# Performance work log

Hardware: AMD Instinct MI355X
Metric: run time of the kernel (lower is better)

The kernel has to match this reference:

```python
import jax, jax.numpy as jnp
import numpy as np

B, T, C = 4, 2048, 2048
H, HD = 16, 128  # n_heads, head_dim; C == H*HD


def _rope_rotate(x, cos, sin):
    """x: [b,t,h,d]; cos/sin: [t, d//2]. Complex multiply on interleaved pairs,
    matching torch view_as_complex on reshape(..., -1, 2)."""
    xr = x[..., 0::2]  # real parts  [b,t,h,d/2]
    xi = x[..., 1::2]  # imag parts
    c = cos[None, :, None, :]
    s = sin[None, :, None, :]
    or_ = xr * c - xi * s
    oi_ = xr * s + xi * c
    # interleave back: [..., d/2, 2] -> [..., d]
    return jnp.stack([or_, oi_], axis=-1).reshape(x.shape)


def setup_inputs() -> dict:
    key = jax.random.key(0)
    ks = jax.random.split(key, 6)
    x = jax.random.normal(ks[0], (B, T, C), dtype=jnp.float32)
    # causal boolean mask: True = attend
    attn_mask = jnp.tril(jnp.ones((T, T), dtype=bool))
    # standard RoPE frequencies (theta=10000)
    inv_freq = 1.0 / (10000.0 ** (np.arange(0, HD, 2, dtype=np.float32) / HD))
    ang = np.arange(T, dtype=np.float32)[:, None] * inv_freq[None, :]  # [T, HD/2]
    rope_cos = jnp.asarray(np.cos(ang))
    rope_sin = jnp.asarray(np.sin(ang))
    sc = 1.0 / np.sqrt(C)
    Wq = jax.random.normal(ks[1], (C, C), dtype=jnp.float32) * sc
    Wk = jax.random.normal(ks[2], (C, C), dtype=jnp.float32) * sc
    Wv = jax.random.normal(ks[3], (C, C), dtype=jnp.float32) * sc
    Wp = jax.random.normal(ks[4], (C, C), dtype=jnp.float32) * sc
    return {"x": x, "attn_mask": attn_mask, "rope_cos": rope_cos,
            "rope_sin": rope_sin, "Wq": Wq, "Wk": Wk, "Wv": Wv, "Wp": Wp}


def reference(x, attn_mask, rope_cos, rope_sin, Wq, Wk, Wv, Wp):
    b, t, c = x.shape
    # QKV projections (nn.Linear: y = x @ W.T), reshape to heads
    q = jnp.einsum('btc,dc->btd', x, Wq).reshape(b, t, H, HD)
    k = jnp.einsum('btc,dc->btd', x, Wk).reshape(b, t, H, HD)
    v = jnp.einsum('btc,dc->btd', x, Wv).reshape(b, t, H, HD)
    # RoPE on q, k
    q = _rope_rotate(q, rope_cos[:t], rope_sin[:t])
    k = _rope_rotate(k, rope_cos[:t], rope_sin[:t])
    # SDPA with boolean mask, scale 1/sqrt(head_dim)
    scores = jnp.einsum('bqhd,bkhd->bhqk', q, k) / jnp.sqrt(jnp.asarray(HD, x.dtype))
    neg = jnp.finfo(scores.dtype).min
    scores = jnp.where(attn_mask[None, None, :t, :t], scores, neg)
    attn = jax.nn.softmax(scores, axis=-1)
    out = jnp.einsum('bhqk,bkhd->bqhd', attn, v).reshape(b, t, H * HD)
    return jnp.einsum('btd,cd->btc', out, Wp)
```

## Files before the change

kernel.cpp:

```cpp
#include <hip/hip_runtime.h>

#define B_    4
#define T_    2048
#define C_    2048
#define H_    16
#define HD_   128
#define LDQK  4096

typedef __attribute__((ext_vector_type(8))) short short8v;
typedef __attribute__((ext_vector_type(4))) float float4v;
typedef __attribute__((ext_vector_type(16))) float float16v;

typedef const __attribute__((address_space(1))) void* gld_src_t;
typedef __attribute__((address_space(3))) void* gld_dst_t;
#define GLDS16(g, l) __builtin_amdgcn_global_load_lds((gld_src_t)(g), (gld_dst_t)(l), 16, 0, 0)

__device__ __forceinline__ unsigned short f2bf(float f) {
  unsigned int u = __float_as_uint(f);
  u += 0x7fffu + ((u >> 16) & 1u);
  return (unsigned short)(u >> 16);
}
__device__ __forceinline__ float bf2f(unsigned short s) {
  return __uint_as_float(((unsigned int)s) << 16);
}
__device__ __forceinline__ unsigned int cvtpk_bf16(float lo, float hi) {
  unsigned int r;
  asm("v_cvt_pk_bf16_f32 %0, %1, %2" : "=v"(r) : "v"(lo), "v"(hi));
  return r;
}

__global__ void cvt_kernel(const float* __restrict__ src, unsigned short* __restrict__ dst, int n4) {
  int i = blockIdx.x * blockDim.x + threadIdx.x;
  if (i >= n4) return;
  float4 v = reinterpret_cast<const float4*>(src)[i];
  ushort4 o;
  o.x = f2bf(v.x); o.y = f2bf(v.y); o.z = f2bf(v.z); o.w = f2bf(v.w);
  reinterpret_cast<ushort4*>(dst)[i] = o;
}


#define ISSUE_HALF(MAT, HA, KT, CBUF)                                             \
  { const unsigned short* gp_ = (MAT) ? Bm : A;                                   \
    const size_t gb_ = (MAT) ? bbase : abase;                                     \
    _Pragma("unroll")                                                             \
    for (int i_ = 0; i_ < 2; ++i_) {                                              \
      int fo_ = (i_ * 512 + tid) * 16;                              \
      int rl_ = fo_ >> 7;                                            \
      int row_ = (HA) * 128 + rl_;                                                \
      int g_ = (fo_ >> 4) & 7;                                                    \
      int ce_ = ((g_ ^ (rl_ & 7)) << 3);              \
      GLDS16(gp_ + gb_ + (size_t)row_ * K + (KT) * 64 + ce_,                      \
             lds + (CBUF) * 65536 + (MAT) * 32768 + (HA) * 16384 + fo_);          \
    } }

#define RD_A(dst, MI, KK, CBUF)                                                   \
  { int row_ = wm * 128 + (MI) * 16 + lr;                                         \
    dst = *reinterpret_cast<const short8v*>(                                      \
        lds + (CBUF) * 65536 + row_ * 128 + (((KK) * 64 + lg * 16) ^ ((row_ & 7) << 4))); }

#define RD_B(dst, NI, KK, CBUF)                                                   \
  { int row_ = wn * 64 + (NI) * 16 + lr;                                          \
    dst = *reinterpret_cast<const short8v*>(                                      \
        lds + (CBUF) * 65536 + 32768 + row_ * 128 + (((KK) * 64 + lg * 16) ^ ((row_ & 7) << 4))); }

#define MFMA_BLOCK(MBASE, BV)                                                     \
  { __builtin_amdgcn_s_setprio(1);                                                \
    _Pragma("unroll")                                                             \
    for (int ni_ = 0; ni_ < 4; ++ni_) {                                           \
      acc[(MBASE)+0][ni_] = __builtin_amdgcn_mfma_f32_16x16x32_bf16(a0, BV[ni_], acc[(MBASE)+0][ni_], 0,0,0); \
      acc[(MBASE)+1][ni_] = __builtin_amdgcn_mfma_f32_16x16x32_bf16(a1, BV[ni_], acc[(MBASE)+1][ni_], 0,0,0); \
      acc[(MBASE)+2][ni_] = __builtin_amdgcn_mfma_f32_16x16x32_bf16(a2, BV[ni_], acc[(MBASE)+2][ni_], 0,0,0); \
      acc[(MBASE)+3][ni_] = __builtin_amdgcn_mfma_f32_16x16x32_bf16(a3, BV[ni_], acc[(MBASE)+3][ni_], 0,0,0); \
    }                                                                             \
    __builtin_amdgcn_s_setprio(0); }

#define FENCE asm volatile("" ::: "memory")

template<int MODE>
__global__ __launch_bounds__(512, 2)
void gemm256(const unsigned short* __restrict__ A, const unsigned short* __restrict__ Bm,
             void* __restrict__ Cout, int K, int NB, int ldc)
{
  extern __shared__ char lds[];
  const int tid = threadIdx.x;
  const int l = tid & 63, w = tid >> 6;
  const int lr = l & 15, lg = l >> 4;
  const int wm = w >> 2, wn = w & 3;

  const int nwg = (int)gridDim.x;
  const int orig = (int)blockIdx.x;
  const int qq = nwg >> 3, rr = nwg & 7;
  const int xcd = orig & 7, idx = orig >> 3;
  const int wg = (xcd < rr ? xcd * (qq + 1) : rr * (qq + 1) + (xcd - rr) * qq) + idx;
  const int bm = wg / NB, bn = wg % NB;

  const size_t abase = (size_t)bm * 256 * (size_t)K;
  const size_t bbase = (size_t)bn * 256 * (size_t)K;

  float4v acc[8][4];
  const float4v fz = {0.f, 0.f, 0.f, 0.f};
#pragma unroll
  for (int i = 0; i < 8; ++i)
#pragma unroll
    for (int j = 0; j < 4; ++j) acc[i][j] = fz;

  const int nk = K >> 6;

  ISSUE_HALF(1, 0, 0, 0)
  ISSUE_HALF(1, 1, 0, 0)
  ISSUE_HALF(0, 0, 0, 0)
  ISSUE_HALF(0, 1, 0, 0)
  ISSUE_HALF(1, 0, (nk > 1 ? 1 : 0), 1)
  asm volatile("s_waitcnt vmcnt(2)" ::: "memory");
  __builtin_amdgcn_s_barrier();
  FENCE;

  short8v a0, a1, a2, a3;
  short8v bv0[4], bv1[4];

  for (int t = 0; t < nk; ++t) {
    const int c = t & 1;
    const int t1 = (t + 1 < nk) ? t + 1 : t;
    const int t2 = (t + 2 < nk) ? t + 2 : t;

    RD_A(a0, 0, 0, c) RD_A(a1, 1, 0, c) RD_A(a2, 2, 0, c) RD_A(a3, 3, 0, c)
    RD_B(bv0[0], 0, 0, c) RD_B(bv0[1], 1, 0, c) RD_B(bv0[2], 2, 0, c) RD_B(bv0[3], 3, 0, c)
    ISSUE_HALF(1, 1, t1, c ^ 1)
    ISSUE_HALF(0, 0, t1, c ^ 1)
    FENCE;
    __builtin_amdgcn_s_barrier();
    MFMA_BLOCK(0, bv0)
    FENCE;
    __builtin_amdgcn_s_barrier();
    FENCE;

    RD_A(a0, 4, 0, c) RD_A(a1, 5, 0, c) RD_A(a2, 6, 0, c) RD_A(a3, 7, 0, c)
    ISSUE_HALF(0, 1, t1, c ^ 1)
    FENCE;
    __builtin_amdgcn_s_barrier();
    MFMA_BLOCK(4, bv0)
    FENCE;
    __builtin_amdgcn_s_barrier();
    FENCE;

    RD_A(a0, 0, 1, c) RD_A(a1, 1, 1, c) RD_A(a2, 2, 1, c) RD_A(a3, 3, 1, c)
    RD_B(bv1[0], 0, 1, c) RD_B(bv1[1], 1, 1, c) RD_B(bv1[2], 2, 1, c) RD_B(bv1[3], 3, 1, c)
    FENCE;
    __builtin_amdgcn_s_barrier();
    MFMA_BLOCK(0, bv1)
    FENCE;
    __builtin_amdgcn_s_barrier();
    FENCE;

    RD_A(a0, 4, 1, c) RD_A(a1, 5, 1, c) RD_A(a2, 6, 1, c) RD_A(a3, 7, 1, c)
    ISSUE_HALF(1, 0, t2, c)
    FENCE;
    __builtin_amdgcn_s_barrier();
    MFMA_BLOCK(4, bv1)
    FENCE;
    asm volatile("s_waitcnt vmcnt(2)" ::: "memory");
    __builtin_amdgcn_s_barrier();
    FENCE;
  }

  const int row0 = bm * 256 + wm * 128;
  const int col0 = bn * 256 + wn * 64;
  if (MODE == 2) {
    unsigned short* vtp = (unsigned short*)Cout;
#pragma unroll
    for (int mi = 0; mi < 8; ++mi)
#pragma unroll
      for (int ni = 0; ni < 4; ++ni) {
        int col = col0 + ni * 16 + lr;
        int hh = col >> 7, dd = col & 127;
        int row = row0 + mi * 16 + lg * 4;
        int bb = row >> 11, t0 = row & 2047;
        ushort4 o4;
        o4.x = f2bf(acc[mi][ni][0]); o4.y = f2bf(acc[mi][ni][1]);
        o4.z = f2bf(acc[mi][ni][2]); o4.w = f2bf(acc[mi][ni][3]);
        *reinterpret_cast<ushort4*>(vtp + (((size_t)(bb * 16 + hh)) << 18) + (((size_t)dd) << 11) + t0) = o4;
      }
  } else {
#pragma unroll
    for (int mi = 0; mi < 8; ++mi)
#pragma unroll
      for (int ni = 0; ni < 4; ++ni)
#pragma unroll
        for (int r2 = 0; r2 < 4; ++r2) {
          int row = row0 + mi * 16 + lg * 4 + r2;
          int col = col0 + ni * 16 + lr;
          float v = acc[mi][ni][r2];
          if (MODE == 1)
            ((unsigned short*)Cout)[(size_t)row * ldc + col] = f2bf(v);
          else
            ((float*)Cout)[(size_t)row * ldc + col] = v;
        }
  }
}

__global__ void rope_kernel(unsigned short* __restrict__ qk,
                            const float* __restrict__ cosb, const float* __restrict__ sinb)
{
  int i = blockIdx.x * blockDim.x + threadIdx.x;
  int seg = i & 15;
  int h   = (i >> 4) & (H_ - 1);
  int bt  = i >> 8;
  if (bt >= B_ * T_) return;
  int t = bt & (T_ - 1);

  float4 cv = *reinterpret_cast<const float4*>(cosb + t * 64 + seg * 4);
  float4 sv = *reinterpret_cast<const float4*>(sinb + t * 64 + seg * 4);
  float cc[4] = {cv.x, cv.y, cv.z, cv.w};
  float ss[4] = {sv.x, sv.y, sv.z, sv.w};

  size_t base = (size_t)bt * LDQK + h * HD_ + seg * 8;
#pragma unroll
  for (int qkx = 0; qkx < 2; ++qkx) {
    unsigned short* p = qk + base + qkx * 2048;
    uint4 u = *reinterpret_cast<uint4*>(p);
    unsigned int* uu = reinterpret_cast<unsigned int*>(&u);
#pragma unroll
    for (int j = 0; j < 4; ++j) {
      float xr = bf2f((unsigned short)(uu[j] & 0xffffu));
      float xi = bf2f((unsigned short)(uu[j] >> 16));
      float orr = xr * cc[j] - xi * ss[j];
      float oii = xr * ss[j] + xi * cc[j];
      uu[j] = (unsigned int)f2bf(orr) | ((unsigned int)f2bf(oii) << 16);
    }
    *reinterpret_cast<uint4*>(p) = u;
  }
}

__global__ __launch_bounds__(256, 2)
void attn_kernel(const unsigned short* __restrict__ qk,
                 const unsigned short* __restrict__ vt,
                 unsigned short* __restrict__ out)
{
  __shared__ unsigned short Kl[2][64 * 128];
  __shared__ unsigned short Vl[2][128 * 64];

  const int wg = (int)blockIdx.x;
  const int bh = ((wg >> 6) << 3) | (wg & 7);
  const int bx = (wg >> 3) & 7;
  const int b = bh >> 4, h = bh & 15;
  const int tid = threadIdx.x, w = tid >> 6, l = tid & 63;
  const int q32 = l & 31, hi = l >> 5;
  const size_t rowbase = (size_t)b * T_;
  const unsigned short* kbase = qk + rowbase * LDQK + 2048 + h * HD_;
  const unsigned short* vbase = vt + (size_t)bh * (HD_ * (size_t)T_);
  const float SC = 0.12754089f;
  const float16v z16 = {0.f,0.f,0.f,0.f,0.f,0.f,0.f,0.f,0.f,0.f,0.f,0.f,0.f,0.f,0.f,0.f};

#define STAGE(kv0_, bi_)                                                          \
  {                                                                               \
    _Pragma("unroll")                                                             \
    for (int i_ = 0; i_ < 4; ++i_) {                                              \
      int fo = (i_ * 256 + tid) * 16;                                             \
      int row = fo >> 8;                                                          \
      int cb = (fo & 255) ^ ((row & 15) << 4);                                    \
      GLDS16(kbase + (size_t)((kv0_) + row) * LDQK + (cb >> 1), (char*)Kl[bi_] + fo); \
    }                                                                             \
    _Pragma("unroll")                                                             \
    for (int i_ = 0; i_ < 4; ++i_) {                                              \
      int fo = (i_ * 256 + tid) * 16;                                             \
      int r6 = (fo >> 8) & 63;                                                    \
      int s_ = (fo >> 7) & 1;                                                     \
      int dd = r6 | ((s_ ^ ((r6 >> 3) & 1)) << 6);                                \
      int k16 = ((fo >> 4) & 7) ^ (dd & 7);                                       \
      GLDS16(vbase + (size_t)dd * T_ + (kv0_) + k16 * 8, (char*)Vl[bi_] + fo);    \
    }                                                                             \
  }

  for (int sel = 0; sel < 2; ++sel) {
    const int qt = sel ? bx : (15 - bx);
    const int q0w = qt * 128 + w * 32;
    const int qg = q0w + q32;

    short8v qf[8];
#pragma unroll
    for (int kf = 0; kf < 8; ++kf) {
      short8v t = *reinterpret_cast<const short8v*>(
          qk + (rowbase + q0w + q32) * (size_t)LDQK + h * HD_ + kf * 16 + hi * 8);
      short8v r;
#pragma unroll
      for (int e = 0; e < 8; ++e) r[e] = (short)f2bf(bf2f((unsigned short)t[e]) * SC);
      qf[kf] = r;
    }

    float16v o[4];
#pragma unroll
    for (int db = 0; db < 4; ++db) o[db] = z16;
    float m_run = -1e30f, lsum = 0.f;

    const int nkv = 2 * (qt + 1);

    STAGE(0, 0);
    __syncthreads();

    for (int tile = 0; tile < nkv; ++tile) {
      const int kv0 = tile * 64;
      const int bi = tile & 1;
      if (tile + 1 < nkv) STAGE((tile + 1) * 64, bi ^ 1);

      if (kv0 <= q0w + 31) {
        float16v stv[2];
        stv[0] = z16; stv[1] = z16;
        __builtin_amdgcn_s_setprio(1);
#pragma unroll
        for (int kb = 0; kb < 2; ++kb) {
          int key = kb * 32 + q32;
          int swz = (key & 15) << 4;
          int rbase = key * 256;
#pragma unroll
          for (int kf = 0; kf < 8; ++kf) {
            short8v ak = *reinterpret_cast<const short8v*>(
                (char*)Kl[bi] + rbase + ((kf * 32 + hi * 16) ^ swz));
            stv[kb] = __builtin_amdgcn_mfma_f32_32x32x16_bf16(ak, qf[kf], stv[kb], 0, 0, 0);
          }
        }
        __builtin_amdgcn_s_setprio(0);
        if (kv0 + 63 > q0w) {
#pragma unroll
          for (int kb = 0; kb < 2; ++kb)
#pragma unroll
            for (int r = 0; r < 16; ++r) {
              int key = kv0 + kb * 32 + (r & 3) + 8 * ((r >> 2) & 3) + 4 * hi;
              if (key > qg) stv[kb][r] = -1e30f;
            }
        }
        float t16[16];
#pragma unroll
        for (int r = 0; r < 16; ++r) t16[r] = fmaxf(stv[0][r], stv[1][r]);
#pragma unroll
        for (int s = 8; s >= 1; s >>= 1)
#pragma unroll
          for (int r = 0; r < s; ++r) t16[r] = fmaxf(t16[r], t16[r + s]);
        float pm = fmaxf(t16[0], __shfl_xor(t16[0], 32));

        if (!__all(pm <= m_run + 8.0f)) {
          float mn = fmaxf(m_run, pm);
          float fac = exp2f(m_run - mn);
          lsum *= fac;
          m_run = mn;
#pragma unroll
          for (int r = 0; r < 16; ++r) {
            int src = (r & 3) + 8 * ((r >> 2) & 3) + 4 * hi;
            float fr = __shfl(fac, src);
#pragma unroll
            for (int db = 0; db < 4; ++db) o[db][r] *= fr;
          }
        }
        {
          float s16[16];
#pragma unroll
          for (int r = 0; r < 16; ++r) {
            float p0 = exp2f(stv[0][r] - m_run);
            float p1 = exp2f(stv[1][r] - m_run);
            stv[0][r] = p0; stv[1][r] = p1;
            s16[r] = p0 + p1;
          }
#pragma unroll
          for (int s = 8; s >= 1; s >>= 1)
#pragma unroll
            for (int r = 0; r < s; ++r) s16[r] += s16[r + s];
          lsum += s16[0] + __shfl_xor(s16[0], 32);
        }
        unsigned int pw0[8], pw1[8], xw0[8], xw1[8];
#pragma unroll
        for (int j = 0; j < 8; ++j) {
          pw0[j] = cvtpk_bf16(stv[0][2 * j], stv[0][2 * j + 1]);
          pw1[j] = cvtpk_bf16(stv[1][2 * j], stv[1][2 * j + 1]);
        }
#pragma unroll
        for (int j = 0; j < 8; ++j) {
          xw0[j] = __shfl_xor(pw0[j], 32);
          xw1[j] = __shfl_xor(pw1[j], 32);
        }
        union UW { unsigned int u[4]; short8v v; };
        short8v pb[4];
        {
          UW a0, a1, c0, c1;
          a0.u[0] = hi ? xw0[2] : pw0[0];  a0.u[1] = hi ? xw0[3] : pw0[1];
          a0.u[2] = hi ? pw0[2] : xw0[0];  a0.u[3] = hi ? pw0[3] : xw0[1];
          a1.u[0] = hi ? xw0[6] : pw0[4];  a1.u[1] = hi ? xw0[7] : pw0[5];
          a1.u[2] = hi ? pw0[6] : xw0[4];  a1.u[3] = hi ? pw0[7] : xw0[5];
          c0.u[0] = hi ? xw1[2] : pw1[0];  c0.u[1] = hi ? xw1[3] : pw1[1];
          c0.u[2] = hi ? pw1[2] : xw1[0];  c0.u[3] = hi ? pw1[3] : xw1[1];
          c1.u[0] = hi ? xw1[6] : pw1[4];  c1.u[1] = hi ? xw1[7] : pw1[5];
          c1.u[2] = hi ? pw1[6] : xw1[4];  c1.u[3] = hi ? pw1[7] : xw1[5];
          pb[0] = a0.v; pb[1] = a1.v; pb[2] = c0.v; pb[3] = c1.v;
        }
        __builtin_amdgcn_s_setprio(1);
#pragma unroll
        for (int db = 0; db < 4; ++db) {
          int dd = db * 32 + q32;
          int rb2 = (dd & 63) * 256 + ((((dd >> 6) ^ ((dd >> 3) & 1)) & 1) << 7);
          int swz = (dd & 7) << 4;
#pragma unroll
          for (int kb16 = 0; kb16 < 4; ++kb16) {
            short8v bv = *reinterpret_cast<const short8v*>(
                (char*)Vl[bi] + rb2 + ((kb16 * 32 + hi * 16) ^ swz));
            o[db] = __builtin_amdgcn_mfma_f32_32x32x16_bf16(pb[kb16], bv, o[db], 0, 0, 0);
          }
        }
        __builtin_amdgcn_s_setprio(0);
      }
      __syncthreads();
    }

    float linv = 1.0f / lsum;
#pragma unroll
    for (int r = 0; r < 16; ++r) {
      int src = (r & 3) + 8 * ((r >> 2) & 3) + 4 * hi;
      float lr_ = __shfl(linv, src);
      size_t rowoff = (rowbase + q0w + src) * (size_t)C_ + h * HD_ + q32;
#pragma unroll
      for (int db = 0; db < 4; ++db)
        out[rowoff + db * 32] = f2bf(o[db][r] * lr_);
    }
  }
#undef STAGE
}

extern "C" void kernel_launch(void* const* d_in, const int* in_sizes, int n_in,
                              void* d_out, int out_size, void* d_ws, size_t ws_size,
                              hipStream_t stream) {
  (void)in_sizes; (void)n_in; (void)out_size; (void)ws_size;
  const float* x  = (const float*)d_in[0];
  const float* rc = (const float*)d_in[2];
  const float* rs = (const float*)d_in[3];
  const float* Wq = (const float*)d_in[4];
  const float* Wk = (const float*)d_in[5];
  const float* Wv = (const float*)d_in[6];
  const float* Wp = (const float*)d_in[7];
  float* outp = (float*)d_out;

  unsigned short* ws    = (unsigned short*)d_ws;
  unsigned short* x_bf  = ws;
  unsigned short* wqkv  = x_bf + 16777216;
  unsigned short* wp_bf = wqkv + 12582912;
  unsigned short* qkbuf = wp_bf + 4194304;
  unsigned short* vtbuf = qkbuf + 33554432;
  unsigned short* ao    = x_bf;

  hipFuncSetAttribute((const void*)gemm256<0>, hipFuncAttributeMaxDynamicSharedMemorySize, 131072);
  hipFuncSetAttribute((const void*)gemm256<1>, hipFuncAttributeMaxDynamicSharedMemorySize, 131072);
  hipFuncSetAttribute((const void*)gemm256<2>, hipFuncAttributeMaxDynamicSharedMemorySize, 131072);

  cvt_kernel<<<16384, 256, 0, stream>>>(x,  x_bf, 4194304);
  cvt_kernel<<<4096,  256, 0, stream>>>(Wq, wqkv,            1048576);
  cvt_kernel<<<4096,  256, 0, stream>>>(Wk, wqkv + 4194304,  1048576);
  cvt_kernel<<<4096,  256, 0, stream>>>(Wv, wqkv + 8388608,  1048576);
  cvt_kernel<<<4096,  256, 0, stream>>>(Wp, wp_bf,           1048576);

  gemm256<1><<<dim3(512), 512, 131072, stream>>>(x_bf, wqkv, qkbuf, 2048, 16, 4096);
  gemm256<2><<<dim3(256), 512, 131072, stream>>>(x_bf, wqkv + 8388608, vtbuf, 2048, 8, 0);

  rope_kernel<<<8192, 256, 0, stream>>>(qkbuf, rc, rs);

  attn_kernel<<<dim3(512), 256, 0, stream>>>(qkbuf, vtbuf, ao);

  gemm256<0><<<dim3(256), 512, 131072, stream>>>(ao, wp_bf, outp, 2048, 8, 2048);
}
```

Baseline: 431.3 us.

## Simplify GEMM main loop to plain double buffering with one barrier per step

Replaces the staggered half-tile prefetch schedule, which had several barriers per K-step and issued one half two steps ahead, with a simple scheme. All four halves of the next tile are issued at the top of each iteration, compute runs without intermediate barriers, and the loop waits for vmcnt(0) plus one barrier at the end. This removes barrier overhead but gives up the finer-grained overlap and the deeper prefetch of the previous schedule, so more global-load latency may be exposed. It also drops the interleaving of LDS reads with the load issue.

```diff
diff --git a/kernel.cpp b/kernel.cpp
--- a/kernel.cpp
+++ b/kernel.cpp
@@ -110,8 +110,7 @@
   ISSUE_HALF(1, 1, 0, 0)
   ISSUE_HALF(0, 0, 0, 0)
   ISSUE_HALF(0, 1, 0, 0)
-  ISSUE_HALF(1, 0, (nk > 1 ? 1 : 0), 1)
-  asm volatile("s_waitcnt vmcnt(2)" ::: "memory");
+  asm volatile("s_waitcnt vmcnt(0)" ::: "memory");
   __builtin_amdgcn_s_barrier();
   FENCE;
 
@@ -120,45 +119,27 @@
 
   for (int t = 0; t < nk; ++t) {
     const int c = t & 1;
-    const int t1 = (t + 1 < nk) ? t + 1 : t;
-    const int t2 = (t + 2 < nk) ? t + 2 : t;
+
+    if (t + 1 < nk) {
+      ISSUE_HALF(1, 0, t + 1, c ^ 1)
+      ISSUE_HALF(1, 1, t + 1, c ^ 1)
+      ISSUE_HALF(0, 0, t + 1, c ^ 1)
+      ISSUE_HALF(0, 1, t + 1, c ^ 1)
+    }
+    FENCE;
 
     RD_A(a0, 0, 0, c) RD_A(a1, 1, 0, c) RD_A(a2, 2, 0, c) RD_A(a3, 3, 0, c)
     RD_B(bv0[0], 0, 0, c) RD_B(bv0[1], 1, 0, c) RD_B(bv0[2], 2, 0, c) RD_B(bv0[3], 3, 0, c)
-    ISSUE_HALF(1, 1, t1, c ^ 1)
-    ISSUE_HALF(0, 0, t1, c ^ 1)
-    FENCE;
-    __builtin_amdgcn_s_barrier();
     MFMA_BLOCK(0, bv0)
-    FENCE;
-    __builtin_amdgcn_s_barrier();
-    FENCE;
-
     RD_A(a0, 4, 0, c) RD_A(a1, 5, 0, c) RD_A(a2, 6, 0, c) RD_A(a3, 7, 0, c)
-    ISSUE_HALF(0, 1, t1, c ^ 1)
-    FENCE;
-    __builtin_amdgcn_s_barrier();
     MFMA_BLOCK(4, bv0)
-    FENCE;
-    __builtin_amdgcn_s_barrier();
-    FENCE;
-
     RD_A(a0, 0, 1, c) RD_A(a1, 1, 1, c) RD_A(a2, 2, 1, c) RD_A(a3, 3, 1, c)
     RD_B(bv1[0], 0, 1, c) RD_B(bv1[1], 1, 1, c) RD_B(bv1[2], 2, 1, c) RD_B(bv1[3], 3, 1, c)
-    FENCE;
-    __builtin_amdgcn_s_barrier();
     MFMA_BLOCK(0, bv1)
-    FENCE;
-    __builtin_amdgcn_s_barrier();
-    FENCE;
-
     RD_A(a0, 4, 1, c) RD_A(a1, 5, 1, c) RD_A(a2, 6, 1, c) RD_A(a3, 7, 1, c)
-    ISSUE_HALF(1, 0, t2, c)
-    FENCE;
-    __builtin_amdgcn_s_barrier();
     MFMA_BLOCK(4, bv1)
-    FENCE;
-    asm volatile("s_waitcnt vmcnt(2)" ::: "memory");
+
+    asm volatile("s_waitcnt vmcnt(0)" ::: "memory");
     __builtin_amdgcn_s_barrier();
     FENCE;
   }
```

Result: no change. 425.6 us (-1.3%).
